# Performance work log

Measured on AMD Instinct MI355X. Metric: run time of the kernel, lower is better.

Reference implementation:

```python
import jax, jax.numpy as jnp
import numpy as np

N_ROW = 50000
N_COL = 50000
E = 600000
D = 128
NEG_SLOPE = 0.01  # torch LeakyReLU default


def _leaky(x):
    return jnp.where(x >= 0, x, NEG_SLOPE * x)


def _mlp(x, W1, b1, W2, b2):
    # (Linear -> LeakyReLU) x2, matching nn.Sequential in Conv_layer
    h = _leaky(x @ W1 + b1)
    return _leaky(h @ W2 + b2)


def setup_inputs() -> dict:
    key = jax.random.key(0)
    ks = jax.random.split(key, 16)
    inp = {
        "feat_row": jax.random.normal(ks[0], (N_ROW, D), jnp.float32),
        "feat_col": jax.random.normal(ks[1], (N_COL, D), jnp.float32),
        "src_c2r": jax.random.randint(ks[2], (E,), 0, N_COL, jnp.int32),
        "dst_c2r": jax.random.randint(ks[3], (E,), 0, N_ROW, jnp.int32),
        "w_c2r": jax.random.uniform(ks[4], (E,), jnp.float32),
        "src_r2c": jax.random.randint(ks[5], (E,), 0, N_ROW, jnp.int32),
        "dst_r2c": jax.random.randint(ks[6], (E,), 0, N_COL, jnp.int32),
        "w_r2c": jax.random.uniform(ks[7], (E,), jnp.float32),
        "W1_c2r": jax.random.normal(ks[8], (D, D), jnp.float32) / np.sqrt(D),
        "b1_c2r": jax.random.normal(ks[9], (D,), jnp.float32) * 0.01,
        "W2_c2r": jax.random.normal(ks[10], (D, D), jnp.float32) / np.sqrt(D),
        "b2_c2r": jax.random.normal(ks[11], (D,), jnp.float32) * 0.01,
        "W1_r2c": jax.random.normal(ks[12], (D, D), jnp.float32) / np.sqrt(D),
        "b1_r2c": jax.random.normal(ks[13], (D,), jnp.float32) * 0.01,
        "W2_r2c": jax.random.normal(ks[14], (D, D), jnp.float32) / np.sqrt(D),
        "b2_r2c": jax.random.normal(ks[15], (D,), jnp.float32) * 0.01,
        "eps_c2r": jnp.zeros((), jnp.float32),  # DGL GINConv init_eps=0
        "eps_r2c": jnp.zeros((), jnp.float32),
    }
    return inp


def reference(feat_row, feat_col, src_c2r, dst_c2r, w_c2r, src_r2c, dst_r2c, w_r2c,
              W1_c2r, b1_c2r, W2_c2r, b2_c2r, W1_r2c, b1_r2c, W2_r2c, b2_r2c,
              eps_c2r, eps_r2c):
    # col -> row GINConv (edge-weighted sum aggregation)
    msg = feat_col[src_c2r] * w_c2r[:, None]                       # [E, D]
    agg_row = jax.ops.segment_sum(msg, dst_c2r, num_segments=N_ROW)
    h_row = _mlp((1.0 + eps_c2r) * feat_row + agg_row, W1_c2r, b1_c2r, W2_c2r, b2_c2r)
    # row -> col GINConv using updated row features
    msg2 = h_row[src_r2c] * w_r2c[:, None]                         # [E, D]
    agg_col = jax.ops.segment_sum(msg2, dst_r2c, num_segments=N_COL)
    h_col = _mlp((1.0 + eps_r2c) * feat_col + agg_col, W1_r2c, b1_r2c, W2_r2c, b2_r2c)
    # residual (use_residual=True): add pre-conv embeddings
    return h_row + feat_row, h_col + feat_col
```

## Files before the change

### kernel.cpp

```cpp
#include <hip/hip_runtime.h>
#include <hip/hip_bf16.h>

#define NROW 50000
#define NCOL 50000
#define DDIM 128
#define CAP  32

typedef __bf16 bf16_t;
typedef __bf16 bf16x2 __attribute__((ext_vector_type(2)));
typedef __bf16 bf16x8 __attribute__((ext_vector_type(8)));
typedef float  f32x4  __attribute__((ext_vector_type(4)));

__device__ __forceinline__ float lrelu(float v) { return v >= 0.f ? v : 0.01f * v; }

__device__ __forceinline__ float ldf(const void* p, size_t i, bool f) {
    return f ? ((const float*)p)[i] : (float)((const bf16_t*)p)[i];
}

__device__ __forceinline__ bool dtf(const int* flags, int fi) {
    return (fi == -1) ? true : (fi == -2) ? false : (flags[fi] != 0);
}

struct TensorTab { const void* p[18]; int n[18]; };

__global__ __launch_bounds__(256) void detect_zero(TensorTab T, int* flags,
                                                   int* z, int zn)
{
    const int tid = threadIdx.x;
    if (blockIdx.x >= 18) {
        int i = (blockIdx.x - 18) * 256 + tid;
        if (i < zn) z[i] = 0;
        return;
    }
    __shared__ int vb, vf;
    const int t = blockIdx.x;
    if (tid == 0) { vb = 0; vf = 0; }
    __syncthreads();
    const int n = T.n[t];
    const bool isFloatArr = (t != 2 && t != 3 && t != 5 && t != 6) && n >= 2;
    if (isFloatArr) {
        int nw = n / 2;
        int wi = (int)(((long long)tid * nw) >> 8);
        unsigned w = ((const unsigned*)T.p[t])[wi];
        unsigned low = w & 0xffffu;
        if (low) {
            int e = (int)((low >> 7) & 0xffu);
            if (e >= 90 && e <= 141) atomicAdd(&vb, 1);
            else                     atomicAdd(&vf, 1);
        }
    }
    __syncthreads();
    if (tid == 0) flags[t] = (isFloatArr && vf > vb) ? 1 : 0;
}

__device__ __forceinline__ void fill_edges(
    int e, const int* __restrict__ dst, const int* __restrict__ srcArr,
    const void* __restrict__ wArr, int nE, int* __restrict__ counts,
    int2* __restrict__ slots2, int* __restrict__ ovCnt,
    int* __restrict__ ovList, bool fW)
{
    if (e >= nE) return;
    int d = dst[e];
    int pos = atomicAdd(&counts[d], 1);
    if (pos < CAP) {
        int2 pk;
        pk.x = srcArr[e];
        pk.y = __float_as_int(ldf(wArr, e, fW));
        slots2[(size_t)d * CAP + pos] = pk;
    } else {
        int k = atomicAdd(ovCnt, 1);
        ovList[k] = e;
    }
}

struct WPtrs { const void* W[4]; int fi[4]; };

__global__ __launch_bounds__(256) void prep_fill(
    WPtrs P, const int* __restrict__ flags, __bf16* __restrict__ wfp,
    const void* __restrict__ feat, __bf16* __restrict__ cbuf, int n8,
    int fiFeat, int cblocks,
    const int* __restrict__ f_dst, const int* __restrict__ f_src,
    const void* __restrict__ f_w, int f_nE, int* __restrict__ f_counts,
    int2* __restrict__ f_slots2, int* __restrict__ f_ovCnt,
    int* __restrict__ f_ovList, int f_fiW)
{
    const int b = blockIdx.x;
    const int tid = threadIdx.x;
    if (b < cblocks) {
        int i = b * 256 + tid;
        if (i >= n8) return;
        const bool f = dtf(flags, fiFeat);
        bf16x8 v;
        if (f) {
            f32x4 a = ((const f32x4*)feat)[i * 2];
            f32x4 c = ((const f32x4*)feat)[i * 2 + 1];
#pragma unroll
            for (int j = 0; j < 4; ++j) { v[j] = (__bf16)a[j]; v[j + 4] = (__bf16)c[j]; }
        } else {
            v = ((const bf16x8*)feat)[i];
        }
        ((bf16x8*)cbuf)[i] = v;
    } else if (b < cblocks + 32) {
        int slot = (b - cblocks) * 256 + tid;
        if (slot >= 4 * 2048) return;
        int m = slot >> 11, sIdx = slot & 2047;
        bool f = flags[P.fi[m]] != 0;
        int l = sIdx & 63, combo = sIdx >> 6;
        int ct = combo >> 2, kk = combo & 3;
        int col  = ct * 16 + (l & 15);
        int krow = kk * 32 + (l >> 4) * 8;
        bf16x8 v;
#pragma unroll
        for (int j = 0; j < 8; ++j)
            v[j] = (__bf16)ldf(P.W[m], (size_t)(krow + j) * DDIM + col, f);
        ((bf16x8*)wfp)[slot] = v;
    } else {
        int e = (b - cblocks - 32) * 256 + tid;
        fill_edges(e, f_dst, f_src, f_w, f_nE, f_counts, f_slots2,
                   f_ovCnt, f_ovList, dtf(flags, f_fiW));
    }
}

__global__ __launch_bounds__(256) void segsum_scan(
    const __bf16* __restrict__ gsrc, const int* __restrict__ counts,
    const int2* __restrict__ slots2, float* __restrict__ agg, int nRows,
    const int* __restrict__ srcArr, const int* __restrict__ dstArr,
    const void* __restrict__ wArr, const int* __restrict__ ovList,
    const int* __restrict__ ovCount, const int* __restrict__ flags, int fiW)
{
    int row = blockIdx.x * 4 + (threadIdx.x >> 6);
    if (row >= nRows) return;
    int lane = threadIdx.x & 63;

    int cntRaw = counts[row];
    int cnt = cntRaw > CAP ? CAP : cntRaw;

    int sr = 0; float wv = 0.f;
    if (lane < cnt) {
        int2 pk = slots2[(size_t)row * CAP + lane];
        sr = pk.x;
        wv = __int_as_float(pk.y);
    }

    float2* ap = (float2*)(agg + (size_t)row * DDIM) + lane;
    float2 acc0 = {0.f, 0.f}, acc1 = {0.f, 0.f};

    const bf16x2* fb = (const bf16x2*)gsrc;
    int i = 0;
    for (; i + 4 <= cnt; i += 4) {
        int   a0 = __shfl(sr, i),     a1 = __shfl(sr, i + 1);
        int   a2 = __shfl(sr, i + 2), a3 = __shfl(sr, i + 3);
        float w0 = __shfl(wv, i),     w1 = __shfl(wv, i + 1);
        float w2 = __shfl(wv, i + 2), w3 = __shfl(wv, i + 3);
        bf16x2 v0 = fb[(size_t)a0 * 64 + lane];
        bf16x2 v1 = fb[(size_t)a1 * 64 + lane];
        bf16x2 v2 = fb[(size_t)a2 * 64 + lane];
        bf16x2 v3 = fb[(size_t)a3 * 64 + lane];
        acc0.x += (float)v0[0] * w0; acc0.y += (float)v0[1] * w0;
        acc1.x += (float)v1[0] * w1; acc1.y += (float)v1[1] * w1;
        acc0.x += (float)v2[0] * w2; acc0.y += (float)v2[1] * w2;
        acc1.x += (float)v3[0] * w3; acc1.y += (float)v3[1] * w3;
    }
    for (; i < cnt; ++i) {
        int   a0 = __shfl(sr, i);
        float w0 = __shfl(wv, i);
        bf16x2 v0 = fb[(size_t)a0 * 64 + lane];
        acc0.x += (float)v0[0] * w0; acc0.y += (float)v0[1] * w0;
    }
    if (cntRaw > CAP) {
        const bool fW = dtf(flags, fiW);
        int nOv = *ovCount;
        for (int k = 0; k < nOv; ++k) {
            int e = ovList[k];
            if (dstArr[e] == row) {
                int s = srcArr[e];
                float wf = ldf(wArr, e, fW);
                bf16x2 v = fb[(size_t)s * 64 + lane];
                acc0.x += (float)v[0] * wf; acc0.y += (float)v[1] * wf;
            }
        }
    }
    acc0.x += acc1.x; acc0.y += acc1.y;
    *ap = acc0;
}

template <bool RESIDUAL, bool HOUT>
__global__ __launch_bounds__(256) void mlp_reg(
    const void* __restrict__ feat, const float* __restrict__ agg,
    const void* __restrict__ b1, const void* __restrict__ b2,
    const void* __restrict__ epsp, float* __restrict__ out, int N,
    const int* __restrict__ flags, int fiFeat, int fiB1, int fiB2, int fiEps,
    const __bf16* __restrict__ pW1, const __bf16* __restrict__ pW2,
    __bf16* __restrict__ hout, int* __restrict__ zc, int zn,
    int mblocks,
    const int* __restrict__ f_dst, const int* __restrict__ f_src,
    const void* __restrict__ f_w, int f_nE, int* __restrict__ f_counts,
    int2* __restrict__ f_slots2, int* __restrict__ f_ovCnt,
    int* __restrict__ f_ovList, int f_fiW)
{
    __shared__ alignas(16) __bf16 h1t[64 * 136];

    const int tid  = threadIdx.x;
    if (f_dst && (int)blockIdx.x >= mblocks) {
        int e = ((int)blockIdx.x - mblocks) * 256 + tid;
        fill_edges(e, f_dst, f_src, f_w, f_nE, f_counts, f_slots2,
                   f_ovCnt, f_ovList, dtf(flags, f_fiW));
        return;
    }
    if (zc) {
        int gi = blockIdx.x * 256 + tid;
        if (gi < zn) zc[gi] = 0;
    }

    const bool fF  = flags[fiFeat] != 0;
    const bool fB1 = flags[fiB1] != 0;
    const bool fB2 = flags[fiB2] != 0;
    const bool fE  = flags[fiEps] != 0;

    const int lane = tid & 63;
    const int wave = tid >> 6;
    const int quad = lane >> 4;
    const int r    = lane & 15;
    const int rowBase = blockIdx.x * 64 + wave * 16;

    const bf16x8* pw1v = (const bf16x8*)pW1;
    bf16x8 w1f[32];
#pragma unroll
    for (int i = 0; i < 32; ++i) w1f[i] = pw1v[i * 64 + lane];

    float bias1[8];
#pragma unroll
    for (int ct = 0; ct < 8; ++ct) bias1[ct] = ldf(b1, ct * 16 + r, fB1);
    const float eps1 = 1.f + ldf(epsp, 0, fE);

    bf16x8 a[4];
    {
        int rowA = rowBase + r;
        if (rowA < N) {
            size_t fb = (size_t)rowA * DDIM + quad * 8;
            const f32x4* gp = (const f32x4*)(agg + fb);
            if (fF) {
                const f32x4* fp = (const f32x4*)((const float*)feat + fb);
#pragma unroll
                for (int kk = 0; kk < 4; ++kk) {
                    f32x4 f0 = fp[kk * 8], f1 = fp[kk * 8 + 1];
                    f32x4 g0 = gp[kk * 8], g1 = gp[kk * 8 + 1];
                    bf16x8 av;
#pragma unroll
                    for (int j = 0; j < 4; ++j) {
                        av[j]     = (__bf16)(f0[j] * eps1 + g0[j]);
                        av[j + 4] = (__bf16)(f1[j] * eps1 + g1[j]);
                    }
                    a[kk] = av;
                }
            } else {
                const bf16x8* fp = (const bf16x8*)((const bf16_t*)feat + fb);
#pragma unroll
                for (int kk = 0; kk < 4; ++kk) {
                    bf16x8 fv = fp[kk * 4];
                    f32x4 g0 = gp[kk * 8], g1 = gp[kk * 8 + 1];
                    bf16x8 av;
#pragma unroll
                    for (int j = 0; j < 4; ++j) {
                        av[j]     = (__bf16)((float)fv[j]     * eps1 + g0[j]);
                        av[j + 4] = (__bf16)((float)fv[j + 4] * eps1 + g1[j]);
                    }
                    a[kk] = av;
                }
            }
        } else {
#pragma unroll
            for (int kk = 0; kk < 4; ++kk)
#pragma unroll
                for (int j = 0; j < 8; ++j) a[kk][j] = (__bf16)0.f;
        }
    }

#pragma unroll
    for (int ct = 0; ct < 8; ++ct) {
        f32x4 acc = {0.f, 0.f, 0.f, 0.f};
#pragma unroll
        for (int kk = 0; kk < 4; ++kk)
            acc = __builtin_amdgcn_mfma_f32_16x16x32_bf16(
                a[kk], w1f[ct * 4 + kk], acc, 0, 0, 0);
#pragma unroll
        for (int gg = 0; gg < 4; ++gg)
            h1t[(wave * 16 + quad * 4 + gg) * 136 + ct * 16 + r] =
                (__bf16)lrelu(acc[gg] + bias1[ct]);
    }

    bf16x8 a2[4];
#pragma unroll
    for (int kk = 0; kk < 4; ++kk)
        a2[kk] = *(const bf16x8*)&h1t[(wave * 16 + r) * 136 + kk * 32 + quad * 8];

    const bf16x8* pw2v = (const bf16x8*)pW2;
    bf16x8 w2f[32];
#pragma unroll
    for (int i = 0; i < 32; ++i) w2f[i] = pw2v[i * 64 + lane];
    float bias2[8];
#pragma unroll
    for (int ct = 0; ct < 8; ++ct) bias2[ct] = ldf(b2, ct * 16 + r, fB2);

#pragma unroll
    for (int ct = 0; ct < 8; ++ct) {
        f32x4 acc = {0.f, 0.f, 0.f, 0.f};
#pragma unroll
        for (int kk = 0; kk < 4; ++kk)
            acc = __builtin_amdgcn_mfma_f32_16x16x32_bf16(
                a2[kk], w2f[ct * 4 + kk], acc, 0, 0, 0);
#pragma unroll
        for (int gg = 0; gg < 4; ++gg) {
            int row = rowBase + quad * 4 + gg;
            float v = lrelu(acc[gg] + bias2[ct]);
            if (HOUT)
                h1t[(wave * 16 + quad * 4 + gg) * 136 + ct * 16 + r] = (__bf16)v;
            if (row < N) {
                int col = ct * 16 + r;
                if (RESIDUAL) v += ldf(feat, (size_t)row * DDIM + col, fF);
                out[(size_t)row * DDIM + col] = v;
            }
        }
    }

    if (HOUT) {
        __syncthreads();
        const int blockBase = blockIdx.x * 64;
#pragma unroll
        for (int c = 0; c < 4; ++c) {
            int chunk = tid + c * 256;
            int row = chunk >> 4;
            int k   = (chunk & 15) * 8;
            if (blockBase + row < N) {
                bf16x8 v = *(const bf16x8*)&h1t[row * 136 + k];
                *(bf16x8*)&hout[(size_t)(blockBase + row) * DDIM + k] = v;
            }
        }
    }
}

__global__ __launch_bounds__(256) void prep_all(
    WPtrs P, const int* __restrict__ flags, __bf16* __restrict__ wfp,
    const void* __restrict__ feat, __bf16* __restrict__ cbuf, int n8, int fiFeat,
    int* __restrict__ zc, int zn, int cblocks, int zblocks)
{
    const int b = blockIdx.x;
    const int tid = threadIdx.x;
    if (b < cblocks) {
        int i = b * 256 + tid;
        if (i >= n8) return;
        const bool f = dtf(flags, fiFeat);
        bf16x8 v;
        if (f) {
            f32x4 a = ((const f32x4*)feat)[i * 2];
            f32x4 c = ((const f32x4*)feat)[i * 2 + 1];
#pragma unroll
            for (int j = 0; j < 4; ++j) { v[j] = (__bf16)a[j]; v[j + 4] = (__bf16)c[j]; }
        } else {
            v = ((const bf16x8*)feat)[i];
        }
        ((bf16x8*)cbuf)[i] = v;
    } else if (b < cblocks + zblocks) {
        int i = (b - cblocks) * 256 + tid;
        if (i < zn) zc[i] = 0;
    } else {
        int slot = (b - cblocks - zblocks) * 256 + tid;
        if (slot >= 4 * 2048) return;
        int m = slot >> 11, sIdx = slot & 2047;
        bool f = flags[P.fi[m]] != 0;
        int l = sIdx & 63, combo = sIdx >> 6;
        int ct = combo >> 2, kk = combo & 3;
        int col  = ct * 16 + (l & 15);
        int krow = kk * 32 + (l >> 4) * 8;
        bf16x8 v;
#pragma unroll
        for (int j = 0; j < 8; ++j)
            v[j] = (__bf16)ldf(P.W[m], (size_t)(krow + j) * DDIM + col, f);
        ((bf16x8*)wfp)[slot] = v;
    }
}

__global__ __launch_bounds__(256) void fill_slots_packed(
    const int* __restrict__ dst, const int* __restrict__ srcArr,
    const void* __restrict__ wArr, int nE, int* __restrict__ counts,
    int2* __restrict__ slots2, int* __restrict__ ovCount,
    int* __restrict__ ovList, float* __restrict__ agg,
    const int* __restrict__ flags, int fiW)
{
    int e = blockIdx.x * 256 + threadIdx.x;
    if (e >= nE) return;
    const bool fW = dtf(flags, fiW);
    int d = dst[e];
    int pos = atomicAdd(&counts[d], 1);
    if (pos < CAP) {
        int2 pk;
        pk.x = srcArr[e];
        pk.y = __float_as_int(ldf(wArr, e, fW));
        slots2[(size_t)d * CAP + pos] = pk;
    } else {
        if (pos == CAP) {
            f32x4 z = {0.f, 0.f, 0.f, 0.f};
            f32x4* rp = (f32x4*)(agg + (size_t)d * DDIM);
#pragma unroll 4
            for (int c = 0; c < DDIM / 4; ++c) rp[c] = z;
        }
        int k = atomicAdd(ovCount, 1);
        ovList[k] = e;
    }
}

__global__ __launch_bounds__(256) void segsum_ov(
    const __bf16* __restrict__ gsrc, const int* __restrict__ counts,
    const int2* __restrict__ slots2, float* __restrict__ agg, int nRows,
    const int* __restrict__ srcArr, const int* __restrict__ dstArr,
    const void* __restrict__ wArr, const int* __restrict__ ovList,
    const int* __restrict__ ovCount, const int* __restrict__ flags, int fiW,
    int gblocks)
{
    const int tid  = threadIdx.x;
    const int lane = tid & 63;

    if ((int)blockIdx.x >= gblocks) {
        const bool fW = dtf(flags, fiW);
        const int nOv = *ovCount;
        const int wv_ = tid >> 6;
        const int nWaves = 64 * 4;
        for (int k = (blockIdx.x - gblocks) * 4 + wv_; k < nOv; k += nWaves) {
            int e = ovList[k];
            int s = srcArr[e], d = dstArr[e];
            float wf = ldf(wArr, e, fW);
            bf16x2 v = ((const bf16x2*)gsrc)[(size_t)s * 64 + lane];
            float* ap = agg + (size_t)d * DDIM + lane * 2;
            unsafeAtomicAdd(ap + 0, (float)v[0] * wf);
            unsafeAtomicAdd(ap + 1, (float)v[1] * wf);
        }
        return;
    }

    int row = blockIdx.x * 4 + (tid >> 6);
    if (row >= nRows) return;

    int cntRaw = counts[row];
    int cnt = cntRaw > CAP ? CAP : cntRaw;

    int sr = 0; float wv = 0.f;
    if (lane < cnt) {
        int2 pk = slots2[(size_t)row * CAP + lane];
        sr = pk.x;
        wv = __int_as_float(pk.y);
    }

    float2* ap = (float2*)(agg + (size_t)row * DDIM) + lane;
    float2 acc0 = {0.f, 0.f}, acc1 = {0.f, 0.f};

    const bf16x2* fb = (const bf16x2*)gsrc;
    int i = 0;
    for (; i + 4 <= cnt; i += 4) {
        int   a0 = __shfl(sr, i),     a1 = __shfl(sr, i + 1);
        int   a2 = __shfl(sr, i + 2), a3 = __shfl(sr, i + 3);
        float w0 = __shfl(wv, i),     w1 = __shfl(wv, i + 1);
        float w2 = __shfl(wv, i + 2), w3 = __shfl(wv, i + 3);
        bf16x2 v0 = fb[(size_t)a0 * 64 + lane];
        bf16x2 v1 = fb[(size_t)a1 * 64 + lane];
        bf16x2 v2 = fb[(size_t)a2 * 64 + lane];
        bf16x2 v3 = fb[(size_t)a3 * 64 + lane];
        acc0.x += (float)v0[0] * w0; acc0.y += (float)v0[1] * w0;
        acc1.x += (float)v1[0] * w1; acc1.y += (float)v1[1] * w1;
        acc0.x += (float)v2[0] * w2; acc0.y += (float)v2[1] * w2;
        acc1.x += (float)v3[0] * w3; acc1.y += (float)v3[1] * w3;
    }
    for (; i < cnt; ++i) {
        int   a0 = __shfl(sr, i);
        float w0 = __shfl(wv, i);
        bf16x2 v0 = fb[(size_t)a0 * 64 + lane];
        acc0.x += (float)v0[0] * w0; acc0.y += (float)v0[1] * w0;
    }
    acc0.x += acc1.x; acc0.y += acc1.y;
    if (cntRaw > CAP) {
        unsafeAtomicAdd(&ap->x, acc0.x);
        unsafeAtomicAdd(&ap->y, acc0.y);
    } else {
        *ap = acc0;
    }
}

__global__ __launch_bounds__(256) void scatter_any(
    const void* __restrict__ feat, const int* __restrict__ src,
    const int* __restrict__ dst, const void* __restrict__ w,
    float* __restrict__ agg, int nE,
    const int* __restrict__ flags, int fiFeat, int fiW)
{
    const bool fF = dtf(flags, fiFeat);
    const bool fW = dtf(flags, fiW);
    int g = blockIdx.x * 256 + threadIdx.x;
    int e = g >> 5;
    if (e >= nE) return;
    int c = (g & 31) << 2;
    int s = src[e], d = dst[e];
    float wf = ldf(w, e, fW);
    size_t base = (size_t)s * DDIM + c;
    float* ap = agg + (size_t)d * DDIM + c;
    unsafeAtomicAdd(ap + 0, ldf(feat, base + 0, fF) * wf);
    unsafeAtomicAdd(ap + 1, ldf(feat, base + 1, fF) * wf);
    unsafeAtomicAdd(ap + 2, ldf(feat, base + 2, fF) * wf);
    unsafeAtomicAdd(ap + 3, ldf(feat, base + 3, fF) * wf);
}

__global__ __launch_bounds__(256) void residual_add(
    float* __restrict__ out, const void* __restrict__ feat, int n4,
    const int* __restrict__ flags, int fiFeat)
{
    const bool fF = flags[fiFeat] != 0;
    int i = blockIdx.x * 256 + threadIdx.x;
    if (i >= n4) return;
    f32x4 o = ((const f32x4*)out)[i];
    f32x4 r;
#pragma unroll
    for (int j = 0; j < 4; ++j) r[j] = o[j] + ldf(feat, (size_t)i * 4 + j, fF);
    ((f32x4*)out)[i] = r;
}

__device__ __forceinline__ void fill_wfrag(const void* __restrict__ W, bool f,
                                           __bf16* wf, int tid)
{
#pragma unroll
    for (int i = 0; i < 8; ++i) {
        int sIdx  = tid + i * 256;
        int l     = sIdx & 63;
        int combo = sIdx >> 6;
        int ct = combo >> 2, kk = combo & 3;
        int col  = ct * 16 + (l & 15);
        int krow = kk * 32 + (l >> 4) * 8;
        __bf16* dp = wf + (size_t)sIdx * 8;
#pragma unroll
        for (int j = 0; j < 8; ++j)
            dp[j] = (__bf16)ldf(W, (size_t)(krow + j) * DDIM + col, f);
    }
}

template <bool RESIDUAL>
__global__ __launch_bounds__(256) void mlp_kernel(
    const void* __restrict__ feat, const float* __restrict__ agg,
    const void* __restrict__ W1, const void* __restrict__ b1,
    const void* __restrict__ W2, const void* __restrict__ b2,
    const void* __restrict__ epsp, float* __restrict__ out, int N,
    const int* __restrict__ flags,
    int fiFeat, int fiW1, int fiB1, int fiW2, int fiB2, int fiEps)
{
    __shared__ alignas(16) __bf16 wf[32 * 64 * 8];
    __shared__ alignas(16) __bf16 h1t[64 * 136];

    const bool fF  = flags[fiFeat] != 0;
    const bool fB1 = flags[fiB1] != 0;
    const bool fB2 = flags[fiB2] != 0;
    const bool fE  = flags[fiEps] != 0;

    const int tid  = threadIdx.x;
    const int lane = tid & 63;
    const int wave = tid >> 6;
    const int quad = lane >> 4;
    const int r    = lane & 15;

    fill_wfrag(W1, flags[fiW1] != 0, wf, tid);

    const float eps1 = 1.f + ldf(epsp, 0, fE);
    const int rowBase = blockIdx.x * 64 + wave * 16;

    bf16x8 a[4];
    {
        int rowA = rowBase + r;
        if (rowA < N) {
            size_t fb = (size_t)rowA * DDIM + quad * 8;
            const f32x4* gp = (const f32x4*)(agg + fb);
            if (fF) {
                const f32x4* fp = (const f32x4*)((const float*)feat + fb);
#pragma unroll
                for (int kk = 0; kk < 4; ++kk) {
                    f32x4 f0 = fp[kk * 8], f1 = fp[kk * 8 + 1];
                    f32x4 g0 = gp[kk * 8], g1 = gp[kk * 8 + 1];
                    bf16x8 av;
#pragma unroll
                    for (int j = 0; j < 4; ++j) {
                        av[j]     = (__bf16)(f0[j] * eps1 + g0[j]);
                        av[j + 4] = (__bf16)(f1[j] * eps1 + g1[j]);
                    }
                    a[kk] = av;
                }
            } else {
                const bf16x8* fp = (const bf16x8*)((const bf16_t*)feat + fb);
#pragma unroll
                for (int kk = 0; kk < 4; ++kk) {
                    bf16x8 fv = fp[kk * 4];
                    f32x4 g0 = gp[kk * 8], g1 = gp[kk * 8 + 1];
                    bf16x8 av;
#pragma unroll
                    for (int j = 0; j < 4; ++j) {
                        av[j]     = (__bf16)((float)fv[j]     * eps1 + g0[j]);
                        av[j + 4] = (__bf16)((float)fv[j + 4] * eps1 + g1[j]);
                    }
                    a[kk] = av;
                }
            }
        } else {
#pragma unroll
            for (int kk = 0; kk < 4; ++kk)
#pragma unroll
                for (int j = 0; j < 8; ++j) a[kk][j] = (__bf16)0.f;
        }
    }

    __syncthreads();

    const bf16x8* wv = (const bf16x8*)wf;
#pragma unroll
    for (int ct = 0; ct < 8; ++ct) {
        f32x4 acc = {0.f, 0.f, 0.f, 0.f};
#pragma unroll
        for (int kk = 0; kk < 4; ++kk)
            acc = __builtin_amdgcn_mfma_f32_16x16x32_bf16(
                a[kk], wv[(ct * 4 + kk) * 64 + lane], acc, 0, 0, 0);
        float bias = ldf(b1, ct * 16 + r, fB1);
#pragma unroll
        for (int gg = 0; gg < 4; ++gg)
            h1t[(wave * 16 + quad * 4 + gg) * 136 + ct * 16 + r] =
                (__bf16)lrelu(acc[gg] + bias);
    }
    __syncthreads();

    bf16x8 a2[4];
#pragma unroll
    for (int kk = 0; kk < 4; ++kk)
        a2[kk] = *(const bf16x8*)&h1t[(wave * 16 + r) * 136 + kk * 32 + quad * 8];

    fill_wfrag(W2, flags[fiW2] != 0, wf, tid);
    __syncthreads();

#pragma unroll
    for (int ct = 0; ct < 8; ++ct) {
        f32x4 acc = {0.f, 0.f, 0.f, 0.f};
#pragma unroll
        for (int kk = 0; kk < 4; ++kk)
            acc = __builtin_amdgcn_mfma_f32_16x16x32_bf16(
                a2[kk], wv[(ct * 4 + kk) * 64 + lane], acc, 0, 0, 0);
        float bias = ldf(b2, ct * 16 + r, fB2);
#pragma unroll
        for (int gg = 0; gg < 4; ++gg) {
            int row = rowBase + quad * 4 + gg;
            if (row < N) {
                int col = ct * 16 + r;
                float v = lrelu(acc[gg] + bias);
                if (RESIDUAL) v += ldf(feat, (size_t)row * DDIM + col, fF);
                out[(size_t)row * DDIM + col] = v;
            }
        }
    }
}

extern "C" void kernel_launch(void* const* d_in, const int* in_sizes, int n_in,
                              void* d_out, int out_size, void* d_ws, size_t ws_size,
                              hipStream_t stream)
{
    const int* src_c2r = (const int*)d_in[2];
    const int* dst_c2r = (const int*)d_in[3];
    const int* src_r2c = (const int*)d_in[5];
    const int* dst_r2c = (const int*)d_in[6];
    const int nE = in_sizes[2];

    char* wsb = (char*)d_ws;
    int*    flags  = (int*)wsb;
    __bf16* wfprep = (__bf16*)(wsb + 128);
    int*    countsA = (int*)(wsb + 128 + 131072);
    int*    ovCntA  = countsA + NROW;
    int*    countsB = countsA + NROW + 8;
    int*    ovCntB  = countsA + 2 * NROW + 8;
    size_t  ofsA2   = 128 + 131072 + ((size_t)2 * NROW + 16) * 4;
    ofsA2 = (ofsA2 + 15) & ~(size_t)15;
    int2*   slots2A2  = (int2*)(wsb + ofsA2);
    size_t  ofsOvA2   = ofsA2 + (size_t)NROW * CAP * 8;
    int*    ovListA2  = (int*)(wsb + ofsOvA2);
    int*    ovListB2  = ovListA2 + nE;
    size_t  ofsCbA2   = (ofsOvA2 + (size_t)nE * 8 + 15) & ~(size_t)15;
    __bf16* cbufA2    = (__bf16*)(wsb + ofsCbA2);
    const size_t NEED_A2 = ofsCbA2 + (size_t)NROW * DDIM * 2;

    int*    counts = (int*)(wsb + 128 + 131072);
    int*    ovCnt  = counts + NROW;
    size_t  ofs    = 128 + 131072 + ((size_t)NROW + 8) * 4;
    ofs = (ofs + 15) & ~(size_t)15;
    int2*   slots2 = (int2*)(wsb + ofs);
    size_t  ofsOvA = ofs + (size_t)NROW * CAP * 8;
    int*    ovListA = (int*)(wsb + ofsOvA);
    size_t  ofsCb  = (ofsOvA + (size_t)nE * 4 + 15) & ~(size_t)15;
    __bf16* cbuf   = (__bf16*)(wsb + ofsCb);
    const size_t NEED_A = ofsCb + (size_t)NROW * DDIM * 2;

    const bool tierA2 = ws_size >= NEED_A2;
    const bool tierA  = ws_size >= NEED_A;

    TensorTab T;
    for (int i = 0; i < 18; ++i) { T.p[i] = d_in[i]; T.n[i] = in_sizes[i]; }

    float* out_row = (float*)d_out;
    float* out_col = out_row + (size_t)NROW * DDIM;
    const size_t aggBytes = (size_t)NROW * DDIM * sizeof(float);

    const int eblocks  = (nE + 255) / 256;
    const int sblocks  = (nE * 32 + 255) / 256;
    const int mblocksR = (NROW + 63) / 64;
    const int mblocksC = (NCOL + 63) / 64;
    const int gblocksR = (NROW + 3) / 4;
    const int gblocksC = (NCOL + 3) / 4;
    const int cblocks  = (NCOL * DDIM / 8 + 255) / 256;

    WPtrs P;
    P.W[0] = d_in[8];  P.fi[0] = 8;
    P.W[1] = d_in[10]; P.fi[1] = 10;
    P.W[2] = d_in[12]; P.fi[2] = 12;
    P.W[3] = d_in[14]; P.fi[3] = 14;

    if (tierA2) {
        const int zn2 = 2 * NROW + 16;
        const int zb2 = (zn2 + 255) / 256;
        detect_zero<<<18 + zb2, 256, 0, stream>>>(T, flags, countsA, zn2);
        prep_fill<<<cblocks + 32 + eblocks, 256, 0, stream>>>(
            P, flags, wfprep, d_in[1], cbufA2, NCOL * DDIM / 8, 1, cblocks,
            dst_c2r, src_c2r, d_in[4], nE, countsA, slots2A2, ovCntA,
            ovListA2, 4);
        segsum_scan<<<gblocksR, 256, 0, stream>>>(cbufA2, countsA, slots2A2,
            out_col, NROW, src_c2r, dst_c2r, d_in[4], ovListA2, ovCntA,
            flags, 4);
        mlp_reg<true, true><<<mblocksR + eblocks, 256, 0, stream>>>(
            d_in[0], out_col, d_in[9], d_in[11], d_in[16],
            out_row, NROW, flags, 0, 9, 11, 16,
            wfprep + 0 * 16384, wfprep + 1 * 16384, cbufA2, nullptr, 0,
            mblocksR, dst_r2c, src_r2c, d_in[7], nE, countsB, slots2A2,
            ovCntB, ovListB2, 7);
        segsum_scan<<<gblocksC, 256, 0, stream>>>(cbufA2, countsB, slots2A2,
            out_col, NCOL, src_r2c, dst_r2c, d_in[7], ovListB2, ovCntB,
            flags, 7);
        mlp_reg<true, false><<<mblocksC, 256, 0, stream>>>(
            d_in[1], out_col, d_in[13], d_in[15], d_in[17],
            out_col, NCOL, flags, 1, 13, 15, 17,
            wfprep + 2 * 16384, wfprep + 3 * 16384, nullptr, nullptr, 0,
            mblocksC, nullptr, nullptr, nullptr, 0, nullptr, nullptr,
            nullptr, nullptr, 0);
    } else if (tierA) {
        const int zblocks = ((NROW + 8) + 255) / 256;
        const int zn      = NROW + 8;
        detect_zero<<<18, 256, 0, stream>>>(T, flags, nullptr, 0);
        prep_all<<<cblocks + zblocks + 32, 256, 0, stream>>>(
            P, flags, wfprep, d_in[1], cbuf, NCOL * DDIM / 8, 1,
            counts, zn, cblocks, zblocks);
        fill_slots_packed<<<eblocks, 256, 0, stream>>>(dst_c2r, src_c2r,
            d_in[4], nE, counts, slots2, ovCnt, ovListA, out_col, flags, 4);
        segsum_ov<<<gblocksR + 64, 256, 0, stream>>>(cbuf, counts, slots2,
            out_col, NROW, src_c2r, dst_c2r, d_in[4], ovListA, ovCnt,
            flags, 4, gblocksR);
        mlp_reg<true, true><<<mblocksR, 256, 0, stream>>>(
            d_in[0], out_col, d_in[9], d_in[11], d_in[16],
            out_row, NROW, flags, 0, 9, 11, 16,
            wfprep + 0 * 16384, wfprep + 1 * 16384, cbuf, counts, zn,
            mblocksR, nullptr, nullptr, nullptr, 0, nullptr, nullptr,
            nullptr, nullptr, 0);
        fill_slots_packed<<<eblocks, 256, 0, stream>>>(dst_r2c, src_r2c,
            d_in[7], nE, counts, slots2, ovCnt, ovListA, out_col, flags, 7);
        segsum_ov<<<gblocksC + 64, 256, 0, stream>>>(cbuf, counts, slots2,
            out_col, NCOL, src_r2c, dst_r2c, d_in[7], ovListA, ovCnt,
            flags, 7, gblocksC);
        mlp_reg<true, false><<<mblocksC, 256, 0, stream>>>(
            d_in[1], out_col, d_in[13], d_in[15], d_in[17],
            out_col, NCOL, flags, 1, 13, 15, 17,
            wfprep + 2 * 16384, wfprep + 3 * 16384, nullptr, nullptr, 0,
            mblocksC, nullptr, nullptr, nullptr, 0, nullptr, nullptr,
            nullptr, nullptr, 0);
    } else {
        detect_zero<<<18, 256, 0, stream>>>(T, flags, nullptr, 0);
        hipMemsetAsync(out_col, 0, aggBytes, stream);
        scatter_any<<<sblocks, 256, 0, stream>>>(d_in[1], src_c2r, dst_c2r,
            d_in[4], out_col, nE, flags, 1, 4);
        mlp_kernel<false><<<mblocksR, 256, 0, stream>>>(
            d_in[0], out_col, d_in[8], d_in[9], d_in[10], d_in[11], d_in[16],
            out_row, NROW, flags, 0, 8, 9, 10, 11, 16);

        hipMemsetAsync(out_col, 0, aggBytes, stream);
        scatter_any<<<sblocks, 256, 0, stream>>>(out_row, src_r2c, dst_r2c,
            d_in[7], out_col, nE, flags, -1, 7);
        residual_add<<<(NROW * DDIM / 4 + 255) / 256, 256, 0, stream>>>(
            out_row, d_in[0], NROW * DDIM / 4, flags, 0);
        mlp_kernel<true><<<mblocksC, 256, 0, stream>>>(
            d_in[1], out_col, d_in[12], d_in[13], d_in[14], d_in[15], d_in[17],
            out_col, NCOL, flags, 1, 12, 13, 14, 15, 17);
    }
}
```

Before: 326.2 us.

## Split MLP work across waves by output column tiles to cut register pressure

Adds an mlp_cs kernel in which each 256-thread block handles 16 rows and each wave computes two 16-column output tiles. The old kernel had every wave hold all 32 W1 and W2 fragments in registers. Input rows are staged cooperatively through LDS with coalesced loads, and hidden activations are shared through LDS behind barriers. The main path now launches this kernel for both MLPs, and the old register-heavy kernel is kept as a separate signature for the fallback tier. The aim is higher occupancy and better load coalescing, at the cost of four times as many blocks, extra syncthreads and repeated weight loads per block.

```diff
diff --git a/kernel.cpp b/kernel.cpp
--- a/kernel.cpp
+++ b/kernel.cpp
@@ -185,32 +185,29 @@
 }
 
 template <bool RESIDUAL, bool HOUT>
-__global__ __launch_bounds__(256) void mlp_reg(
+__global__ __launch_bounds__(256) void mlp_cs(
     const void* __restrict__ feat, const float* __restrict__ agg,
     const void* __restrict__ b1, const void* __restrict__ b2,
     const void* __restrict__ epsp, float* __restrict__ out, int N,
     const int* __restrict__ flags, int fiFeat, int fiB1, int fiB2, int fiEps,
     const __bf16* __restrict__ pW1, const __bf16* __restrict__ pW2,
-    __bf16* __restrict__ hout, int* __restrict__ zc, int zn,
+    __bf16* __restrict__ hout,
     int mblocks,
     const int* __restrict__ f_dst, const int* __restrict__ f_src,
     const void* __restrict__ f_w, int f_nE, int* __restrict__ f_counts,
     int2* __restrict__ f_slots2, int* __restrict__ f_ovCnt,
     int* __restrict__ f_ovList, int f_fiW)
 {
-    __shared__ alignas(16) __bf16 h1t[64 * 136];
-
-    const int tid  = threadIdx.x;
+    __shared__ alignas(16) __bf16 At[16 * 136];
+    __shared__ alignas(16) __bf16 H1[16 * 136];
+
+    const int tid = threadIdx.x;
     if (f_dst && (int)blockIdx.x >= mblocks) {
         int e = ((int)blockIdx.x - mblocks) * 256 + tid;
         fill_edges(e, f_dst, f_src, f_w, f_nE, f_counts, f_slots2,
                    f_ovCnt, f_ovList, dtf(flags, f_fiW));
         return;
     }
-    if (zc) {
-        int gi = blockIdx.x * 256 + tid;
-        if (gi < zn) zc[gi] = 0;
-    }
 
     const bool fF  = flags[fiFeat] != 0;
     const bool fB1 = flags[fiB1] != 0;
@@ -221,100 +218,108 @@
     const int wave = tid >> 6;
     const int quad = lane >> 4;
     const int r    = lane & 15;
-    const int rowBase = blockIdx.x * 64 + wave * 16;
-
-    const bf16x8* pw1v = (const bf16x8*)pW1;
-    bf16x8 w1f[32];
-#pragma unroll
-    for (int i = 0; i < 32; ++i) w1f[i] = pw1v[i * 64 + lane];
-
-    float bias1[8];
-#pragma unroll
-    for (int ct = 0; ct < 8; ++ct) bias1[ct] = ldf(b1, ct * 16 + r, fB1);
+    const int rowBase = blockIdx.x * 16;
     const float eps1 = 1.f + ldf(epsp, 0, fE);
 
-    bf16x8 a[4];
     {
-        int rowA = rowBase + r;
-        if (rowA < N) {
-            size_t fb = (size_t)rowA * DDIM + quad * 8;
-            const f32x4* gp = (const f32x4*)(agg + fb);
+        int row = tid >> 4;
+        int k0  = (tid & 15) * 8;
+        int g   = rowBase + row;
+        bf16x8 av;
+        if (g < N) {
+            size_t base = (size_t)g * DDIM + k0;
+            const f32x4* gp = (const f32x4*)(agg + base);
+            f32x4 g0 = gp[0], g1 = gp[1];
             if (fF) {
-                const f32x4* fp = (const f32x4*)((const float*)feat + fb);
-#pragma unroll
-                for (int kk = 0; kk < 4; ++kk) {
-                    f32x4 f0 = fp[kk * 8], f1 = fp[kk * 8 + 1];
-                    f32x4 g0 = gp[kk * 8], g1 = gp[kk * 8 + 1];
-                    bf16x8 av;
-#pragma unroll
-                    for (int j = 0; j < 4; ++j) {
-                        av[j]     = (__bf16)(f0[j] * eps1 + g0[j]);
-                        av[j + 4] = (__bf16)(f1[j] * eps1 + g1[j]);
-                    }
-                    a[kk] = av;
+                const f32x4* fp = (const f32x4*)((const float*)feat + base);
+                f32x4 f0 = fp[0], f1 = fp[1];
+#pragma unroll
+                for (int j = 0; j < 4; ++j) {
+                    av[j]     = (__bf16)(f0[j] * eps1 + g0[j]);
+                    av[j + 4] = (__bf16)(f1[j] * eps1 + g1[j]);
                 }
             } else {
-                const bf16x8* fp = (const bf16x8*)((const bf16_t*)feat + fb);
-#pragma unroll
-                for (int kk = 0; kk < 4; ++kk) {
-                    bf16x8 fv = fp[kk * 4];
-                    f32x4 g0 = gp[kk * 8], g1 = gp[kk * 8 + 1];
-                    bf16x8 av;
-#pragma unroll
-                    for (int j = 0; j < 4; ++j) {
-                        av[j]     = (__bf16)((float)fv[j]     * eps1 + g0[j]);
-                        av[j + 4] = (__bf16)((float)fv[j + 4] * eps1 + g1[j]);
-                    }
-                    a[kk] = av;
+                bf16x8 fv = *(const bf16x8*)((const bf16_t*)feat + base);
+#pragma unroll
+                for (int j = 0; j < 4; ++j) {
+                    av[j]     = (__bf16)((float)fv[j]     * eps1 + g0[j]);
+                    av[j + 4] = (__bf16)((float)fv[j + 4] * eps1 + g1[j]);
                 }
             }
         } else {
 #pragma unroll
-            for (int kk = 0; kk < 4; ++kk)
-#pragma unroll
-                for (int j = 0; j < 8; ++j) a[kk][j] = (__bf16)0.f;
-        }
-    }
-
-#pragma unroll
-    for (int ct = 0; ct < 8; ++ct) {
+            for (int j = 0; j < 8; ++j) av[j] = (__bf16)0.f;
+        }
+        *(bf16x8*)&At[row * 136 + k0] = av;
+    }
+    __syncthreads();
+
+    bf16x8 a[4];
+#pragma unroll
+    for (int kk = 0; kk < 4; ++kk)
+        a[kk] = *(const bf16x8*)&At[r * 136 + kk * 32 + quad * 8];
+
+    const int ct0 = wave * 2, ct1 = ct0 + 1;
+
+    const bf16x8* pw1v = (const bf16x8*)pW1;
+    bf16x8 wfa[4], wfb[4];
+#pragma unroll
+    for (int kk = 0; kk < 4; ++kk) {
+        wfa[kk] = pw1v[(ct0 * 4 + kk) * 64 + lane];
+        wfb[kk] = pw1v[(ct1 * 4 + kk) * 64 + lane];
+    }
+    float b1a = ldf(b1, ct0 * 16 + r, fB1);
+    float b1b = ldf(b1, ct1 * 16 + r, fB1);
+
+    {
+        f32x4 acc = {0.f, 0.f, 0.f, 0.f};
+#pragma unroll
+        for (int kk = 0; kk < 4; ++kk)
+            acc = __builtin_amdgcn_mfma_f32_16x16x32_bf16(a[kk], wfa[kk], acc, 0, 0, 0);
+#pragma unroll
+        for (int gg = 0; gg < 4; ++gg)
+            H1[(quad * 4 + gg) * 136 + ct0 * 16 + r] = (__bf16)lrelu(acc[gg] + b1a);
+    }
+    {
+        f32x4 acc = {0.f, 0.f, 0.f, 0.f};
+#pragma unroll
+        for (int kk = 0; kk < 4; ++kk)
+            acc = __builtin_amdgcn_mfma_f32_16x16x32_bf16(a[kk], wfb[kk], acc, 0, 0, 0);
+#pragma unroll
+        for (int gg = 0; gg < 4; ++gg)
+            H1[(quad * 4 + gg) * 136 + ct1 * 16 + r] = (__bf16)lrelu(acc[gg] + b1b);
+    }
+    __syncthreads();
+
+    bf16x8 a2[4];
+#pragma unroll
+    for (int kk = 0; kk < 4; ++kk)
+        a2[kk] = *(const bf16x8*)&H1[r * 136 + kk * 32 + quad * 8];
+
+    const bf16x8* pw2v = (const bf16x8*)pW2;
+#pragma unroll
+    for (int kk = 0; kk < 4; ++kk) {
+        wfa[kk] = pw2v[(ct0 * 4 + kk) * 64 + lane];
+        wfb[kk] = pw2v[(ct1 * 4 + kk) * 64 + lane];
+    }
+    float b2a = ldf(b2, ct0 * 16 + r, fB2);
+    float b2b = ldf(b2, ct1 * 16 + r, fB2);
+
+#pragma unroll
+    for (int cp = 0; cp < 2; ++cp) {
+        const int ct = cp ? ct1 : ct0;
         f32x4 acc = {0.f, 0.f, 0.f, 0.f};
 #pragma unroll
         for (int kk = 0; kk < 4; ++kk)
             acc = __builtin_amdgcn_mfma_f32_16x16x32_bf16(
-                a[kk], w1f[ct * 4 + kk], acc, 0, 0, 0);
-#pragma unroll
-        for (int gg = 0; gg < 4; ++gg)
-            h1t[(wave * 16 + quad * 4 + gg) * 136 + ct * 16 + r] =
-                (__bf16)lrelu(acc[gg] + bias1[ct]);
-    }
-
-    bf16x8 a2[4];
-#pragma unroll
-    for (int kk = 0; kk < 4; ++kk)
-        a2[kk] = *(const bf16x8*)&h1t[(wave * 16 + r) * 136 + kk * 32 + quad * 8];
-
-    const bf16x8* pw2v = (const bf16x8*)pW2;
-    bf16x8 w2f[32];
-#pragma unroll
-    for (int i = 0; i < 32; ++i) w2f[i] = pw2v[i * 64 + lane];
-    float bias2[8];
-#pragma unroll
-    for (int ct = 0; ct < 8; ++ct) bias2[ct] = ldf(b2, ct * 16 + r, fB2);
-
-#pragma unroll
-    for (int ct = 0; ct < 8; ++ct) {
-        f32x4 acc = {0.f, 0.f, 0.f, 0.f};
-#pragma unroll
-        for (int kk = 0; kk < 4; ++kk)
-            acc = __builtin_amdgcn_mfma_f32_16x16x32_bf16(
-                a2[kk], w2f[ct * 4 + kk], acc, 0, 0, 0);
+                a2[kk], cp ? wfb[kk] : wfa[kk], acc, 0, 0, 0);
+        float bias = cp ? b2b : b2a;
 #pragma unroll
         for (int gg = 0; gg < 4; ++gg) {
             int row = rowBase + quad * 4 + gg;
-            float v = lrelu(acc[gg] + bias2[ct]);
+            float v = lrelu(acc[gg] + bias);
             if (HOUT)
-                h1t[(wave * 16 + quad * 4 + gg) * 136 + ct * 16 + r] = (__bf16)v;
+                At[(quad * 4 + gg) * 136 + ct * 16 + r] = (__bf16)v;
             if (row < N) {
                 int col = ct * 16 + r;
                 if (RESIDUAL) v += ldf(feat, (size_t)row * DDIM + col, fF);
@@ -325,17 +330,12 @@
 
     if (HOUT) {
         __syncthreads();
-        const int blockBase = blockIdx.x * 64;
-#pragma unroll
-        for (int c = 0; c < 4; ++c) {
-            int chunk = tid + c * 256;
-            int row = chunk >> 4;
-            int k   = (chunk & 15) * 8;
-            if (blockBase + row < N) {
-                bf16x8 v = *(const bf16x8*)&h1t[row * 136 + k];
-                *(bf16x8*)&hout[(size_t)(blockBase + row) * DDIM + k] = v;
-            }
-        }
+        int row = tid >> 4;
+        int k0  = (tid & 15) * 8;
+        int g   = rowBase + row;
+        if (g < N)
+            *(bf16x8*)&hout[(size_t)g * DDIM + k0] =
+                *(const bf16x8*)&At[row * 136 + k0];
     }
 }
 
@@ -484,6 +484,150 @@
     }
 }
 
+template <bool RESIDUAL, bool HOUT>
+__global__ __launch_bounds__(256) void mlp_reg(
+    const void* __restrict__ feat, const float* __restrict__ agg,
+    const void* __restrict__ b1, const void* __restrict__ b2,
+    const void* __restrict__ epsp, float* __restrict__ out, int N,
+    const int* __restrict__ flags, int fiFeat, int fiB1, int fiB2, int fiEps,
+    const __bf16* __restrict__ pW1, const __bf16* __restrict__ pW2,
+    __bf16* __restrict__ hout, int* __restrict__ zc, int zn)
+{
+    __shared__ alignas(16) __bf16 h1t[64 * 136];
+
+    const int tid  = threadIdx.x;
+    if (zc) {
+        int gi = blockIdx.x * 256 + tid;
+        if (gi < zn) zc[gi] = 0;
+    }
+
+    const bool fF  = flags[fiFeat] != 0;
+    const bool fB1 = flags[fiB1] != 0;
+    const bool fB2 = flags[fiB2] != 0;
+    const bool fE  = flags[fiEps] != 0;
+
+    const int lane = tid & 63;
+    const int wave = tid >> 6;
+    const int quad = lane >> 4;
+    const int r    = lane & 15;
+    const int rowBase = blockIdx.x * 64 + wave * 16;
+
+    const bf16x8* pw1v = (const bf16x8*)pW1;
+    bf16x8 w1f[32];
+#pragma unroll
+    for (int i = 0; i < 32; ++i) w1f[i] = pw1v[i * 64 + lane];
+
+    float bias1[8];
+#pragma unroll
+    for (int ct = 0; ct < 8; ++ct) bias1[ct] = ldf(b1, ct * 16 + r, fB1);
+    const float eps1 = 1.f + ldf(epsp, 0, fE);
+
+    bf16x8 a[4];
+    {
+        int rowA = rowBase + r;
+        if (rowA < N) {
+            size_t fb = (size_t)rowA * DDIM + quad * 8;
+            const f32x4* gp = (const f32x4*)(agg + fb);
+            if (fF) {
+                const f32x4* fp = (const f32x4*)((const float*)feat + fb);
+#pragma unroll
+                for (int kk = 0; kk < 4; ++kk) {
+                    f32x4 f0 = fp[kk * 8], f1 = fp[kk * 8 + 1];
+                    f32x4 g0 = gp[kk * 8], g1 = gp[kk * 8 + 1];
+                    bf16x8 av;
+#pragma unroll
+                    for (int j = 0; j < 4; ++j) {
+                        av[j]     = (__bf16)(f0[j] * eps1 + g0[j]);
+                        av[j + 4] = (__bf16)(f1[j] * eps1 + g1[j]);
+                    }
+                    a[kk] = av;
+                }
+            } else {
+                const bf16x8* fp = (const bf16x8*)((const bf16_t*)feat + fb);
+#pragma unroll
+                for (int kk = 0; kk < 4; ++kk) {
+                    bf16x8 fv = fp[kk * 4];
+                    f32x4 g0 = gp[kk * 8], g1 = gp[kk * 8 + 1];
+                    bf16x8 av;
+#pragma unroll
+                    for (int j = 0; j < 4; ++j) {
+                        av[j]     = (__bf16)((float)fv[j]     * eps1 + g0[j]);
+                        av[j + 4] = (__bf16)((float)fv[j + 4] * eps1 + g1[j]);
+                    }
+                    a[kk] = av;
+                }
+            }
+        } else {
+#pragma unroll
+            for (int kk = 0; kk < 4; ++kk)
+#pragma unroll
+                for (int j = 0; j < 8; ++j) a[kk][j] = (__bf16)0.f;
+        }
+    }
+
+#pragma unroll
+    for (int ct = 0; ct < 8; ++ct) {
+        f32x4 acc = {0.f, 0.f, 0.f, 0.f};
+#pragma unroll
+        for (int kk = 0; kk < 4; ++kk)
+            acc = __builtin_amdgcn_mfma_f32_16x16x32_bf16(
+                a[kk], w1f[ct * 4 + kk], acc, 0, 0, 0);
+#pragma unroll
+        for (int gg = 0; gg < 4; ++gg)
+            h1t[(wave * 16 + quad * 4 + gg) * 136 + ct * 16 + r] =
+                (__bf16)lrelu(acc[gg] + bias1[ct]);
+    }
+
+    bf16x8 a2[4];
+#pragma unroll
+    for (int kk = 0; kk < 4; ++kk)
+        a2[kk] = *(const bf16x8*)&h1t[(wave * 16 + r) * 136 + kk * 32 + quad * 8];
+
+    const bf16x8* pw2v = (const bf16x8*)pW2;
+    bf16x8 w2f[32];
+#pragma unroll
+    for (int i = 0; i < 32; ++i) w2f[i] = pw2v[i * 64 + lane];
+    float bias2[8];
+#pragma unroll
+    for (int ct = 0; ct < 8; ++ct) bias2[ct] = ldf(b2, ct * 16 + r, fB2);
+
+#pragma unroll
+    for (int ct = 0; ct < 8; ++ct) {
+        f32x4 acc = {0.f, 0.f, 0.f, 0.f};
+#pragma unroll
+        for (int kk = 0; kk < 4; ++kk)
+            acc = __builtin_amdgcn_mfma_f32_16x16x32_bf16(
+                a2[kk], w2f[ct * 4 + kk], acc, 0, 0, 0);
+#pragma unroll
+        for (int gg = 0; gg < 4; ++gg) {
+            int row = rowBase + quad * 4 + gg;
+            float v = lrelu(acc[gg] + bias2[ct]);
+            if (HOUT)
+                h1t[(wave * 16 + quad * 4 + gg) * 136 + ct * 16 + r] = (__bf16)v;
+            if (row < N) {
+                int col = ct * 16 + r;
+                if (RESIDUAL) v += ldf(feat, (size_t)row * DDIM + col, fF);
+                out[(size_t)row * DDIM + col] = v;
+            }
+        }
+    }
+
+    if (HOUT) {
+        __syncthreads();
+        const int blockBase = blockIdx.x * 64;
+#pragma unroll
+        for (int c = 0; c < 4; ++c) {
+            int chunk = tid + c * 256;
+            int row = chunk >> 4;
+            int k   = (chunk & 15) * 8;
+            if (blockBase + row < N) {
+                bf16x8 v = *(const bf16x8*)&h1t[row * 136 + k];
+                *(bf16x8*)&hout[(size_t)(blockBase + row) * DDIM + k] = v;
+            }
+        }
+    }
+}
+
 __global__ __launch_bounds__(256) void scatter_any(
     const void* __restrict__ feat, const int* __restrict__ src,
     const int* __restrict__ dst, const void* __restrict__ w,
@@ -708,6 +852,8 @@
     const int sblocks  = (nE * 32 + 255) / 256;
     const int mblocksR = (NROW + 63) / 64;
     const int mblocksC = (NCOL + 63) / 64;
+    const int csR      = (NROW + 15) / 16;
+    const int csC      = (NCOL + 15) / 16;
     const int gblocksR = (NROW + 3) / 4;
     const int gblocksC = (NCOL + 3) / 4;
     const int cblocks  = (NCOL * DDIM / 8 + 255) / 256;
@@ -729,20 +875,20 @@
         segsum_scan<<<gblocksR, 256, 0, stream>>>(cbufA2, countsA, slots2A2,
             out_col, NROW, src_c2r, dst_c2r, d_in[4], ovListA2, ovCntA,
             flags, 4);
-        mlp_reg<true, true><<<mblocksR + eblocks, 256, 0, stream>>>(
+        mlp_cs<true, true><<<csR + eblocks, 256, 0, stream>>>(
             d_in[0], out_col, d_in[9], d_in[11], d_in[16],
             out_row, NROW, flags, 0, 9, 11, 16,
-            wfprep + 0 * 16384, wfprep + 1 * 16384, cbufA2, nullptr, 0,
-            mblocksR, dst_r2c, src_r2c, d_in[7], nE, countsB, slots2A2,
+            wfprep + 0 * 16384, wfprep + 1 * 16384, cbufA2,
+            csR, dst_r2c, src_r2c, d_in[7], nE, countsB, slots2A2,
             ovCntB, ovListB2, 7);
         segsum_scan<<<gblocksC, 256, 0, stream>>>(cbufA2, countsB, slots2A2,
             out_col, NCOL, src_r2c, dst_r2c, d_in[7], ovListB2, ovCntB,
             flags, 7);
-        mlp_reg<true, false><<<mblocksC, 256, 0, stream>>>(
+        mlp_cs<true, false><<<csC, 256, 0, stream>>>(
             d_in[1], out_col, d_in[13], d_in[15], d_in[17],
             out_col, NCOL, flags, 1, 13, 15, 17,
-            wfprep + 2 * 16384, wfprep + 3 * 16384, nullptr, nullptr, 0,
-            mblocksC, nullptr, nullptr, nullptr, 0, nullptr, nullptr,
+            wfprep + 2 * 16384, wfprep + 3 * 16384, nullptr,
+            csC, nullptr, nullptr, nullptr, 0, nullptr, nullptr,
             nullptr, nullptr, 0);
     } else if (tierA) {
         const int zblocks = ((NROW + 8) + 255) / 256;
@@ -759,9 +905,7 @@
         mlp_reg<true, true><<<mblocksR, 256, 0, stream>>>(
             d_in[0], out_col, d_in[9], d_in[11], d_in[16],
             out_row, NROW, flags, 0, 9, 11, 16,
-            wfprep + 0 * 16384, wfprep + 1 * 16384, cbuf, counts, zn,
-            mblocksR, nullptr, nullptr, nullptr, 0, nullptr, nullptr,
-            nullptr, nullptr, 0);
+            wfprep + 0 * 16384, wfprep + 1 * 16384, cbuf, counts, zn);
         fill_slots_packed<<<eblocks, 256, 0, stream>>>(dst_r2c, src_r2c,
             d_in[7], nE, counts, slots2, ovCnt, ovListA, out_col, flags, 7);
         segsum_ov<<<gblocksC + 64, 256, 0, stream>>>(cbuf, counts, slots2,
@@ -770,9 +914,7 @@
         mlp_reg<true, false><<<mblocksC, 256, 0, stream>>>(
             d_in[1], out_col, d_in[13], d_in[15], d_in[17],
             out_col, NCOL, flags, 1, 13, 15, 17,
-            wfprep + 2 * 16384, wfprep + 3 * 16384, nullptr, nullptr, 0,
-            mblocksC, nullptr, nullptr, nullptr, 0, nullptr, nullptr,
-            nullptr, nullptr, 0);
+            wfprep + 2 * 16384, wfprep + 3 * 16384, nullptr, nullptr, 0);
     } else {
         detect_zero<<<18, 256, 0, stream>>>(T, flags, nullptr, 0);
         hipMemsetAsync(out_col, 0, aggBytes, stream);
```

Result: faster. 309.5 us (-5.1%).
